# Performance work log

Measured on AMD Instinct MI355X. Metric: run time of the kernel, lower is better.

## Reference

```python
import jax, jax.numpy as jnp
import numpy as np

DIM = 256

def setup_inputs() -> dict:
    key = jax.random.key(0)
    ks = jax.random.split(key, 7)
    x = jax.random.normal(ks[0], (4, 4096, DIM), dtype=jnp.float32)
    s = 1.0 / np.sqrt(DIM)
    Wq = jax.random.uniform(ks[1], (DIM, DIM), jnp.float32, -s, s)
    Wk = jax.random.uniform(ks[2], (DIM, DIM), jnp.float32, -s, s)
    Wv = jax.random.uniform(ks[3], (DIM, DIM), jnp.float32, -s, s)
    bq = jax.random.uniform(ks[4], (DIM,), jnp.float32, -s, s)
    bk = jax.random.uniform(ks[5], (DIM,), jnp.float32, -s, s)
    bv = jax.random.uniform(ks[6], (DIM,), jnp.float32, -s, s)
    return {"x": x, "Wq": Wq, "bq": bq, "Wk": Wk, "bk": bk, "Wv": Wv, "bv": bv}

def reference(x, Wq, bq, Wk, bk, Wv, bv):
    # torch Linear: y = x @ W.T + b
    q = jnp.einsum('bsd,ed->bse', x, Wq) + bq
    k = jnp.einsum('bsd,ed->bse', x, Wk) + bk
    v = jnp.einsum('bsd,ed->bse', x, Wv) + bv
    scale = 1.0 / jnp.sqrt(jnp.float32(x.shape[-1]))
    scores = jnp.einsum('bse,bte->bst', q, k) * scale  # [B,S,S]
    weights = jax.nn.softmax(scores, axis=-1)
    return jnp.einsum('bst,bte->bse', weights, v)
```

## Files before the change

### kernel.cpp

```cpp
#include <hip/hip_runtime.h>

#define BB 4
#define SS 4096
#define DD 256
#define NS 4
#define BS (BB*SS)
#define KT 32
#define QT 128
#define RW 32
#define NITER ((SS/NS)/KT)

typedef _Float16 f16x8 __attribute__((ext_vector_type(8)));
typedef _Float16 f16x4 __attribute__((ext_vector_type(4)));
typedef float f32x4 __attribute__((ext_vector_type(4)));

union b32tof16x8 { int i[4]; f16x8 v; };

__device__ __forceinline__ void gl2lds16(const void* g, void* l) {
    __builtin_amdgcn_global_load_lds(
        (const __attribute__((address_space(1))) void*)g,
        (__attribute__((address_space(3))) void*)l, 16, 0, 0);
}

__global__ __launch_bounds__(256) void wconv_kernel(
    const float* __restrict__ Wq, const float* __restrict__ Wk,
    const float* __restrict__ Wv, _Float16* __restrict__ wh)
{
    const int p = blockIdx.y;
    const float* W = (p == 0) ? Wq : (p == 1) ? Wk : Wv;
    _Float16* dst = wh + (size_t)p * DD * DD;
    const int i = (blockIdx.x * 256 + threadIdx.x) * 4;
    const float4 v = ((const float4*)W)[i >> 2];
    f16x4 h;
    h[0] = (_Float16)v.x; h[1] = (_Float16)v.y;
    h[2] = (_Float16)v.z; h[3] = (_Float16)v.w;
    *(f16x4*)(dst + i) = h;
}

__global__ __launch_bounds__(256) void proj_kernel(
    const float* __restrict__ x, const _Float16* __restrict__ wh,
    const float* __restrict__ bq, const float* __restrict__ bk,
    const float* __restrict__ bv,
    _Float16* __restrict__ qh, _Float16* __restrict__ kh,
    _Float16* __restrict__ vt)
{
    __shared__ _Float16 smem[19000];
    _Float16* xs = smem;
    _Float16* xp = smem + 16384;

    const int tid = threadIdx.x;
    const int p   = blockIdx.y;
    const int b   = blockIdx.x >> 6;
    const int s0  = (blockIdx.x & 63) * 64;
    const float* xb = x + ((size_t)b * SS + s0) * DD;

#pragma unroll
    for (int i = 0; i < 16; ++i) {
        int f4 = i * 256 + tid;
        int row = f4 >> 6, c4 = f4 & 63;
        const float4 v = ((const float4*)(xb + (size_t)row * DD))[c4];
        f16x4 h;
        h[0] = (_Float16)v.x; h[1] = (_Float16)v.y;
        h[2] = (_Float16)v.z; h[3] = (_Float16)v.w;
        *(f16x4*)(&xs[row * 264 + c4 * 4]) = h;
    }
    __syncthreads();

    const int wv   = tid >> 6;
    const int lane = tid & 63;
    const int lo   = lane & 15;
    const int quad = lane >> 4;

    f16x8 afr[8];
#pragma unroll
    for (int ks = 0; ks < 8; ++ks)
        afr[ks] = *(const f16x8*)(&xs[(wv * 16 + lo) * 264 + ks * 32 + quad * 8]);
    __syncthreads();

    const _Float16* W  = wh + (size_t)p * DD * DD;
    const float*    bi = (p == 0) ? bq : (p == 1) ? bk : bv;
    const float     mulv = (p == 0) ? (0.0625f * 1.44269504088896340736f) : 1.0f;

    auto stage_w = [&](int c, _Float16* ws) {
#pragma unroll
        for (int i = 0; i < 4; ++i) {
            const int flat = i * 256 + tid;
            const int e  = flat >> 5;
            const int ps = flat & 31;
            const int cg = ps ^ (e & 15);
            gl2lds16(W + (size_t)(c * 32 + e) * DD + cg * 8, ws + flat * 8);
        }
    };

    stage_w(0, smem);

    for (int c = 0; c < 8; ++c) {
        __syncthreads();
        if (c + 1 < 8) stage_w(c + 1, smem + ((c + 1) & 1) * 8192);
        const _Float16* ws = smem + (c & 1) * 8192;

        f32x4 acc[2];
        acc[0] = (f32x4){0.f, 0.f, 0.f, 0.f};
        acc[1] = (f32x4){0.f, 0.f, 0.f, 0.f};
#pragma unroll
        for (int ks = 0; ks < 8; ++ks) {
            const int g = (ks * 4 + quad) ^ lo;
            f16x8 b0 = *(const f16x8*)(ws + (lo) * 256 + g * 8);
            f16x8 b1 = *(const f16x8*)(ws + (16 + lo) * 256 + g * 8);
            acc[0] = __builtin_amdgcn_mfma_f32_16x16x32_f16(afr[ks], b0, acc[0], 0, 0, 0);
            acc[1] = __builtin_amdgcn_mfma_f32_16x16x32_f16(afr[ks], b1, acc[1], 0, 0, 0);
        }

        if (p < 2) {
            _Float16* xw = xp + wv * 640;
#pragma unroll
            for (int ntl = 0; ntl < 2; ++ntl) {
                const float bias = bi[c * 32 + ntl * 16 + lo];
#pragma unroll
                for (int r = 0; r < 4; ++r)
                    xw[(quad * 4 + r) * 40 + ntl * 16 + lo] =
                        (_Float16)((acc[ntl][r] + bias) * mulv);
            }
            _Float16* dstb = (p == 0 ? qh : kh)
                + ((size_t)b * SS + s0 + wv * 16) * DD + c * 32;
            const int row = lane >> 2, g = lane & 3;
            f16x8 v = *(const f16x8*)(xw + row * 40 + g * 8);
            *(f16x8*)(dstb + (size_t)row * DD + g * 8) = v;
        } else {
#pragma unroll
            for (int ntl = 0; ntl < 2; ++ntl) {
                const int e = c * 32 + ntl * 16 + lo;
                const float bias = bi[e];
                f16x4 pk;
#pragma unroll
                for (int r = 0; r < 4; ++r) pk[r] = (_Float16)(acc[ntl][r] + bias);
                *(f16x4*)(vt + ((size_t)b * DD + e) * SS + s0 + wv * 16 + quad * 4) = pk;
            }
        }
    }
}

__device__ __forceinline__ void stage_kv(
    const _Float16* kb_g, const _Float16* vb_g, int t0,
    _Float16* kt, _Float16* vt_l, int wv, int lane)
{
#pragma unroll
    for (int i = 0; i < 4; ++i) {
        const int kb = wv * 4 + i;
        {
            const int r  = kb * 2 + (lane >> 5);
            const int ps = lane & 31;
            const int cg = ps ^ (r & 15);
            gl2lds16(kb_g + (size_t)(t0 + r) * DD + cg * 8, kt + kb * 512);
        }
        {
            const int r  = kb * 16 + (lane >> 2);
            const int ps = lane & 3;
            const int cg = ps ^ ((r >> 1) & 3);
            gl2lds16(vb_g + (size_t)r * SS + t0 + cg * 8, vt_l + kb * 512);
        }
    }
}

__global__ __launch_bounds__(256, 2) void attn_kernel(
    const _Float16* __restrict__ qh, const _Float16* __restrict__ kh,
    const _Float16* __restrict__ vt, _Float16* __restrict__ part,
    float* __restrict__ ml)
{
    __shared__ _Float16 kt_s[2][KT * DD];
    __shared__ _Float16 vt_s[2][DD * KT];

    const int tid  = threadIdx.x;
    const int wv   = tid >> 6;
    const int lane = tid & 63;
    const int lo   = lane & 15;
    const int quad = lane >> 4;

    const int combo = blockIdx.x & 15;
    const int qt    = blockIdx.x >> 4;
    const int b     = combo >> 2;
    const int split = combo & 3;

    const int qrow0 = qt * QT + wv * RW;
    const _Float16* qbase = qh + ((size_t)b * SS + qrow0) * DD;

    f16x8 qf[2][8];
#pragma unroll
    for (int ntq = 0; ntq < 2; ++ntq)
#pragma unroll
        for (int ks = 0; ks < 8; ++ks)
            qf[ntq][ks] = *(const f16x8*)(qbase + (size_t)(ntq * 16 + lo) * DD + ks * 32 + quad * 8);

    f32x4 acco[2][16];
#pragma unroll
    for (int ntq = 0; ntq < 2; ++ntq)
#pragma unroll
        for (int i = 0; i < 16; ++i) acco[ntq][i] = (f32x4){0.f, 0.f, 0.f, 0.f};
    float l_lane[2] = {0.f, 0.f};

    const _Float16* kbase = kh + (size_t)b * SS * DD;
    const _Float16* vbase = vt + (size_t)b * DD * SS;
    const int tbeg = split * (SS / NS);

    const int addrA = (((quad & 1) << 5) + lo) << 2;
    const int addrB = addrA + 64;

    stage_kv(kbase, vbase, tbeg, kt_s[0], vt_s[0], wv, lane);

    for (int it = 0; it < NITER; ++it) {
        const int cur = it & 1;
        __syncthreads();
        if (it + 1 < NITER)
            stage_kv(kbase, vbase, tbeg + (it + 1) * KT,
                     kt_s[cur ^ 1], vt_s[cur ^ 1], wv, lane);

        const _Float16* kt = kt_s[cur];
        const _Float16* vv = vt_s[cur];

        f32x4 st[2][2];
#pragma unroll
        for (int i = 0; i < 2; ++i)
#pragma unroll
            for (int j = 0; j < 2; ++j) st[i][j] = (f32x4){0.f, 0.f, 0.f, 0.f};
#pragma unroll
        for (int ks = 0; ks < 8; ++ks)
#pragma unroll
            for (int ntk = 0; ntk < 2; ++ntk) {
                f16x8 kfr = *(const f16x8*)(
                    &kt[(ntk * 16 + lo) * DD + ((ks * 4 + quad) ^ lo) * 8]);
                st[ntk][0] = __builtin_amdgcn_mfma_f32_16x16x32_f16(kfr, qf[0][ks], st[ntk][0], 0, 0, 0);
                st[ntk][1] = __builtin_amdgcn_mfma_f32_16x16x32_f16(kfr, qf[1][ks], st[ntk][1], 0, 0, 0);
            }

        int ipk[2][2][2];
#pragma unroll
        for (int ntk = 0; ntk < 2; ++ntk)
#pragma unroll
            for (int ntq = 0; ntq < 2; ++ntq) {
                const float p0 = exp2f(st[ntk][ntq][0]);
                const float p1 = exp2f(st[ntk][ntq][1]);
                const float p2 = exp2f(st[ntk][ntq][2]);
                const float p3 = exp2f(st[ntk][ntq][3]);
                l_lane[ntq] += (p0 + p1) + (p2 + p3);
                ipk[ntk][ntq][0] = __builtin_bit_cast(int, __builtin_amdgcn_cvt_pkrtz(p0, p1));
                ipk[ntk][ntq][1] = __builtin_bit_cast(int, __builtin_amdgcn_cvt_pkrtz(p2, p3));
            }

        f16x8 bP[2];
        const bool hi = (quad >= 2);
#pragma unroll
        for (int ntq = 0; ntq < 2; ++ntq) {
            int j01a = __builtin_amdgcn_ds_bpermute(addrA, ipk[0][ntq][0]);
            int j01b = __builtin_amdgcn_ds_bpermute(addrA, ipk[1][ntq][0]);
            int j23a = __builtin_amdgcn_ds_bpermute(addrA, ipk[0][ntq][1]);
            int j23b = __builtin_amdgcn_ds_bpermute(addrA, ipk[1][ntq][1]);
            int j45a = __builtin_amdgcn_ds_bpermute(addrB, ipk[0][ntq][0]);
            int j45b = __builtin_amdgcn_ds_bpermute(addrB, ipk[1][ntq][0]);
            int j67a = __builtin_amdgcn_ds_bpermute(addrB, ipk[0][ntq][1]);
            int j67b = __builtin_amdgcn_ds_bpermute(addrB, ipk[1][ntq][1]);
            b32tof16x8 u;
            u.i[0] = hi ? j01b : j01a;
            u.i[1] = hi ? j23b : j23a;
            u.i[2] = hi ? j45b : j45a;
            u.i[3] = hi ? j67b : j67a;
            bP[ntq] = u.v;
        }

#pragma unroll
        for (int nte = 0; nte < 16; ++nte) {
            f16x8 vfr = *(const f16x8*)(
                &vv[(nte * 16 + lo) * 32 + (quad ^ ((lo >> 1) & 3)) * 8]);
            acco[0][nte] = __builtin_amdgcn_mfma_f32_16x16x32_f16(vfr, bP[0], acco[0][nte], 0, 0, 0);
            acco[1][nte] = __builtin_amdgcn_mfma_f32_16x16x32_f16(vfr, bP[1], acco[1][nte], 0, 0, 0);
        }
    }

    const int growb = b * SS + qt * QT + wv * RW;
    _Float16* ph = part + (size_t)split * BS * DD;
#pragma unroll
    for (int ntq = 0; ntq < 2; ++ntq) {
        const int row = growb + ntq * 16 + lo;
#pragma unroll
        for (int nte = 0; nte < 16; ++nte) {
            f16x4 pk;
#pragma unroll
            for (int r = 0; r < 4; ++r) pk[r] = (_Float16)acco[ntq][nte][r];
            *(f16x4*)(ph + (size_t)row * DD + nte * 16 + quad * 4) = pk;
        }
    }
#pragma unroll
    for (int ntq = 0; ntq < 2; ++ntq) {
        float l = l_lane[ntq];
        l += __shfl_xor(l, 16, 64);
        l += __shfl_xor(l, 32, 64);
        if (quad == 0)
            ml[(size_t)split * BS + growb + ntq * 16 + lo] = l;
    }
}

__global__ __launch_bounds__(256) void combine_kernel(
    const _Float16* __restrict__ part, const float* __restrict__ ml,
    float* __restrict__ out)
{
    const int row = blockIdx.x * 4 + (threadIdx.x >> 6);
    const int e4  = threadIdx.x & 63;

    float lsum = 0.f;
#pragma unroll
    for (int i = 0; i < NS; ++i) lsum += ml[(size_t)i * BS + row];
    const float inv = 1.f / lsum;

    float o0 = 0.f, o1 = 0.f, o2 = 0.f, o3 = 0.f;
#pragma unroll
    for (int i = 0; i < NS; ++i) {
        const f16x4 pv = ((const f16x4*)(part + ((size_t)i * BS + row) * DD))[e4];
        o0 += (float)pv[0]; o1 += (float)pv[1];
        o2 += (float)pv[2]; o3 += (float)pv[3];
    }
    float4 o = {o0 * inv, o1 * inv, o2 * inv, o3 * inv};
    ((float4*)(out + (size_t)row * DD))[e4] = o;
}

extern "C" void kernel_launch(void* const* d_in, const int* in_sizes, int n_in,
                              void* d_out, int out_size, void* d_ws, size_t ws_size,
                              hipStream_t stream) {
    const float* x  = (const float*)d_in[0];
    const float* Wq = (const float*)d_in[1];
    const float* bq = (const float*)d_in[2];
    const float* Wk = (const float*)d_in[3];
    const float* bk = (const float*)d_in[4];
    const float* Wv = (const float*)d_in[5];
    const float* bv = (const float*)d_in[6];
    float* out = (float*)d_out;

    _Float16* qh = (_Float16*)d_ws;
    _Float16* kh = qh + (size_t)BS * DD;
    _Float16* vt = kh + (size_t)BS * DD;
    _Float16* wh = vt + (size_t)BS * DD;
    _Float16* part = wh + (size_t)3 * DD * DD;
    float* ml = (float*)(part + (size_t)NS * BS * DD);

    wconv_kernel<<<dim3(64, 3), dim3(256), 0, stream>>>(Wq, Wk, Wv, wh);
    proj_kernel<<<dim3(BS / 64, 3), dim3(256), 0, stream>>>(
        x, wh, bq, bk, bv, qh, kh, vt);
    attn_kernel<<<dim3((SS / QT) * 16), dim3(256), 0, stream>>>(
        qh, kh, vt, part, ml);
    combine_kernel<<<dim3(BS / 4), dim3(256), 0, stream>>>(part, ml, out);
}
```

Measured before the change: 188.0 us.

## Store Q/K in FP8 and use fp8 MFMA for scores with larger query tiles

Q and K are quantized to FP8 in the projection kernel, and the QK^T score MFMAs switch to the fp8 16x16x32 instruction, which halves K staging bytes and Q register footprint. The softmax scale moves from the projection into the exp2 argument. The query tile doubles to 64 rows per wave (NTQ=4), so each K/V tile staged in LDS is reused across more queries, with occupancy lowered to one block per SM in launch bounds. This risks accuracy loss from FP8 scores and register pressure or lower occupancy from the larger accumulator set.

```diff
diff --git a/kernel.cpp b/kernel.cpp
--- a/kernel.cpp
+++ b/kernel.cpp
@@ -6,13 +6,15 @@
 #define NS 4
 #define BS (BB*SS)
 #define KT 32
-#define QT 128
-#define RW 32
+#define QT 256
+#define RW 64
+#define NTQ 4
 #define NITER ((SS/NS)/KT)
 
 typedef _Float16 f16x8 __attribute__((ext_vector_type(8)));
 typedef _Float16 f16x4 __attribute__((ext_vector_type(4)));
 typedef float f32x4 __attribute__((ext_vector_type(4)));
+typedef unsigned char u8;
 
 union b32tof16x8 { int i[4]; f16x8 v; };
 
@@ -41,8 +43,7 @@
     const float* __restrict__ x, const _Float16* __restrict__ wh,
     const float* __restrict__ bq, const float* __restrict__ bk,
     const float* __restrict__ bv,
-    _Float16* __restrict__ qh, _Float16* __restrict__ kh,
-    _Float16* __restrict__ vt)
+    u8* __restrict__ qh, u8* __restrict__ kh, _Float16* __restrict__ vt)
 {
     __shared__ _Float16 smem[19000];
     _Float16* xs = smem;
@@ -79,7 +80,6 @@
 
     const _Float16* W  = wh + (size_t)p * DD * DD;
     const float*    bi = (p == 0) ? bq : (p == 1) ? bk : bv;
-    const float     mulv = (p == 0) ? (0.0625f * 1.44269504088896340736f) : 1.0f;
 
     auto stage_w = [&](int c, _Float16* ws) {
 #pragma unroll
@@ -119,13 +119,18 @@
 #pragma unroll
                 for (int r = 0; r < 4; ++r)
                     xw[(quad * 4 + r) * 40 + ntl * 16 + lo] =
-                        (_Float16)((acc[ntl][r] + bias) * mulv);
+                        (_Float16)(acc[ntl][r] + bias);
             }
-            _Float16* dstb = (p == 0 ? qh : kh)
-                + ((size_t)b * SS + s0 + wv * 16) * DD + c * 32;
             const int row = lane >> 2, g = lane & 3;
             f16x8 v = *(const f16x8*)(xw + row * 40 + g * 8);
-            *(f16x8*)(dstb + (size_t)row * DD + g * 8) = v;
+            int w0 = __builtin_amdgcn_cvt_pk_fp8_f32((float)v[0], (float)v[1], 0, false);
+            w0     = __builtin_amdgcn_cvt_pk_fp8_f32((float)v[2], (float)v[3], w0, true);
+            int w1 = __builtin_amdgcn_cvt_pk_fp8_f32((float)v[4], (float)v[5], 0, false);
+            w1     = __builtin_amdgcn_cvt_pk_fp8_f32((float)v[6], (float)v[7], w1, true);
+            int2 pkw = {w0, w1};
+            u8* dstb = (p == 0 ? qh : kh)
+                + ((size_t)b * SS + s0 + wv * 16 + row) * DD + c * 32 + g * 8;
+            *(int2*)dstb = pkw;
         } else {
 #pragma unroll
             for (int ntl = 0; ntl < 2; ++ntl) {
@@ -141,33 +146,34 @@
 }
 
 __device__ __forceinline__ void stage_kv(
-    const _Float16* kb_g, const _Float16* vb_g, int t0,
-    _Float16* kt, _Float16* vt_l, int wv, int lane)
-{
+    const u8* kb_g, const _Float16* vb_g, int t0,
+    u8* kt, _Float16* vt_l, int wv, int lane)
+{
+#pragma unroll
+    for (int i = 0; i < 2; ++i) {
+        const int slotb = (wv * 2 + i) * 64;
+        const int slot  = slotb + lane;
+        const int r  = slot >> 4;
+        const int ps = slot & 15;
+        const int cg = ps ^ (r & 15);
+        gl2lds16(kb_g + (size_t)(t0 + r) * DD + cg * 16, kt + slotb * 16);
+    }
 #pragma unroll
     for (int i = 0; i < 4; ++i) {
         const int kb = wv * 4 + i;
-        {
-            const int r  = kb * 2 + (lane >> 5);
-            const int ps = lane & 31;
-            const int cg = ps ^ (r & 15);
-            gl2lds16(kb_g + (size_t)(t0 + r) * DD + cg * 8, kt + kb * 512);
-        }
-        {
-            const int r  = kb * 16 + (lane >> 2);
-            const int ps = lane & 3;
-            const int cg = ps ^ ((r >> 1) & 3);
-            gl2lds16(vb_g + (size_t)r * SS + t0 + cg * 8, vt_l + kb * 512);
-        }
-    }
-}
-
-__global__ __launch_bounds__(256, 2) void attn_kernel(
-    const _Float16* __restrict__ qh, const _Float16* __restrict__ kh,
+        const int r  = kb * 16 + (lane >> 2);
+        const int ps = lane & 3;
+        const int cg = ps ^ ((r >> 1) & 3);
+        gl2lds16(vb_g + (size_t)r * SS + t0 + cg * 8, vt_l + kb * 512);
+    }
+}
+
+__global__ __launch_bounds__(256, 1) void attn_kernel(
+    const u8* __restrict__ qh, const u8* __restrict__ kh,
     const _Float16* __restrict__ vt, _Float16* __restrict__ part,
     float* __restrict__ ml)
 {
-    __shared__ _Float16 kt_s[2][KT * DD];
+    __shared__ u8       kt_s[2][KT * DD];
     __shared__ _Float16 vt_s[2][DD * KT];
 
     const int tid  = threadIdx.x;
@@ -182,25 +188,28 @@
     const int split = combo & 3;
 
     const int qrow0 = qt * QT + wv * RW;
-    const _Float16* qbase = qh + ((size_t)b * SS + qrow0) * DD;
-
-    f16x8 qf[2][8];
-#pragma unroll
-    for (int ntq = 0; ntq < 2; ++ntq)
+    const u8* qbase = qh + ((size_t)b * SS + qrow0) * DD;
+
+    long qf[NTQ][8];
+#pragma unroll
+    for (int ntq = 0; ntq < NTQ; ++ntq)
 #pragma unroll
         for (int ks = 0; ks < 8; ++ks)
-            qf[ntq][ks] = *(const f16x8*)(qbase + (size_t)(ntq * 16 + lo) * DD + ks * 32 + quad * 8);
-
-    f32x4 acco[2][16];
-#pragma unroll
-    for (int ntq = 0; ntq < 2; ++ntq)
+            qf[ntq][ks] = *(const long*)(qbase + (size_t)(ntq * 16 + lo) * DD + ks * 32 + quad * 8);
+
+    f32x4 acco[NTQ][16];
+#pragma unroll
+    for (int ntq = 0; ntq < NTQ; ++ntq)
 #pragma unroll
         for (int i = 0; i < 16; ++i) acco[ntq][i] = (f32x4){0.f, 0.f, 0.f, 0.f};
-    float l_lane[2] = {0.f, 0.f};
-
-    const _Float16* kbase = kh + (size_t)b * SS * DD;
+    float l_lane[NTQ];
+#pragma unroll
+    for (int ntq = 0; ntq < NTQ; ++ntq) l_lane[ntq] = 0.f;
+
+    const u8*       kbase = kh + (size_t)b * SS * DD;
     const _Float16* vbase = vt + (size_t)b * DD * SS;
     const int tbeg = split * (SS / NS);
+    const float SCL = 0.0625f * 1.44269504088896340736f;
 
     const int addrA = (((quad & 1) << 5) + lo) << 2;
     const int addrB = addrA + 64;
@@ -214,42 +223,45 @@
             stage_kv(kbase, vbase, tbeg + (it + 1) * KT,
                      kt_s[cur ^ 1], vt_s[cur ^ 1], wv, lane);
 
-        const _Float16* kt = kt_s[cur];
+        const u8*       kt = kt_s[cur];
         const _Float16* vv = vt_s[cur];
 
-        f32x4 st[2][2];
+        f32x4 st[2][NTQ];
 #pragma unroll
         for (int i = 0; i < 2; ++i)
 #pragma unroll
-            for (int j = 0; j < 2; ++j) st[i][j] = (f32x4){0.f, 0.f, 0.f, 0.f};
+            for (int j = 0; j < NTQ; ++j) st[i][j] = (f32x4){0.f, 0.f, 0.f, 0.f};
 #pragma unroll
         for (int ks = 0; ks < 8; ++ks)
 #pragma unroll
             for (int ntk = 0; ntk < 2; ++ntk) {
-                f16x8 kfr = *(const f16x8*)(
-                    &kt[(ntk * 16 + lo) * DD + ((ks * 4 + quad) ^ lo) * 8]);
-                st[ntk][0] = __builtin_amdgcn_mfma_f32_16x16x32_f16(kfr, qf[0][ks], st[ntk][0], 0, 0, 0);
-                st[ntk][1] = __builtin_amdgcn_mfma_f32_16x16x32_f16(kfr, qf[1][ks], st[ntk][1], 0, 0, 0);
+                const int R  = ntk * 16 + lo;
+                const int ps = (ks * 2 + (quad >> 1)) ^ lo;
+                long kfr = *(const long*)(kt + R * 256 + ps * 16 + (quad & 1) * 8);
+#pragma unroll
+                for (int ntq = 0; ntq < NTQ; ++ntq)
+                    st[ntk][ntq] = __builtin_amdgcn_mfma_f32_16x16x32_fp8_fp8(
+                        kfr, qf[ntq][ks], st[ntk][ntq], 0, 0, 0);
             }
 
-        int ipk[2][2][2];
+        int ipk[2][NTQ][2];
 #pragma unroll
         for (int ntk = 0; ntk < 2; ++ntk)
 #pragma unroll
-            for (int ntq = 0; ntq < 2; ++ntq) {
-                const float p0 = exp2f(st[ntk][ntq][0]);
-                const float p1 = exp2f(st[ntk][ntq][1]);
-                const float p2 = exp2f(st[ntk][ntq][2]);
-                const float p3 = exp2f(st[ntk][ntq][3]);
+            for (int ntq = 0; ntq < NTQ; ++ntq) {
+                const float p0 = exp2f(st[ntk][ntq][0] * SCL);
+                const float p1 = exp2f(st[ntk][ntq][1] * SCL);
+                const float p2 = exp2f(st[ntk][ntq][2] * SCL);
+                const float p3 = exp2f(st[ntk][ntq][3] * SCL);
                 l_lane[ntq] += (p0 + p1) + (p2 + p3);
                 ipk[ntk][ntq][0] = __builtin_bit_cast(int, __builtin_amdgcn_cvt_pkrtz(p0, p1));
                 ipk[ntk][ntq][1] = __builtin_bit_cast(int, __builtin_amdgcn_cvt_pkrtz(p2, p3));
             }
 
-        f16x8 bP[2];
+        f16x8 bP[NTQ];
         const bool hi = (quad >= 2);
 #pragma unroll
-        for (int ntq = 0; ntq < 2; ++ntq) {
+        for (int ntq = 0; ntq < NTQ; ++ntq) {
             int j01a = __builtin_amdgcn_ds_bpermute(addrA, ipk[0][ntq][0]);
             int j01b = __builtin_amdgcn_ds_bpermute(addrA, ipk[1][ntq][0]);
             int j23a = __builtin_amdgcn_ds_bpermute(addrA, ipk[0][ntq][1]);
@@ -270,15 +282,17 @@
         for (int nte = 0; nte < 16; ++nte) {
             f16x8 vfr = *(const f16x8*)(
                 &vv[(nte * 16 + lo) * 32 + (quad ^ ((lo >> 1) & 3)) * 8]);
-            acco[0][nte] = __builtin_amdgcn_mfma_f32_16x16x32_f16(vfr, bP[0], acco[0][nte], 0, 0, 0);
-            acco[1][nte] = __builtin_amdgcn_mfma_f32_16x16x32_f16(vfr, bP[1], acco[1][nte], 0, 0, 0);
+#pragma unroll
+            for (int ntq = 0; ntq < NTQ; ++ntq)
+                acco[ntq][nte] = __builtin_amdgcn_mfma_f32_16x16x32_f16(
+                    vfr, bP[ntq], acco[ntq][nte], 0, 0, 0);
         }
     }
 
     const int growb = b * SS + qt * QT + wv * RW;
     _Float16* ph = part + (size_t)split * BS * DD;
 #pragma unroll
-    for (int ntq = 0; ntq < 2; ++ntq) {
+    for (int ntq = 0; ntq < NTQ; ++ntq) {
         const int row = growb + ntq * 16 + lo;
 #pragma unroll
         for (int nte = 0; nte < 16; ++nte) {
@@ -289,7 +303,7 @@
         }
     }
 #pragma unroll
-    for (int ntq = 0; ntq < 2; ++ntq) {
+    for (int ntq = 0; ntq < NTQ; ++ntq) {
         float l = l_lane[ntq];
         l += __shfl_xor(l, 16, 64);
         l += __shfl_xor(l, 32, 64);
@@ -333,9 +347,9 @@
     const float* bv = (const float*)d_in[6];
     float* out = (float*)d_out;
 
-    _Float16* qh = (_Float16*)d_ws;
-    _Float16* kh = qh + (size_t)BS * DD;
-    _Float16* vt = kh + (size_t)BS * DD;
+    u8* qh = (u8*)d_ws;
+    u8* kh = qh + (size_t)BS * DD;
+    _Float16* vt = (_Float16*)(kh + (size_t)BS * DD);
     _Float16* wh = vt + (size_t)BS * DD;
     _Float16* part = wh + (size_t)3 * DD * DD;
     float* ml = (float*)(part + (size_t)NS * BS * DD);
```

After: 207.6 us. +10.4%, slower.
